# Kernel tuning notes

Measured on AMD Instinct MI355X. Metric: run time of the kernel, lower is better.

Reference implementation:

```python
import jax, jax.numpy as jnp
import numpy as np
from jax.scipy.special import xlogy

NUM_TTA = 64
FILTER_VIEWS = 0.1
KEPT_VIEWS = int(FILTER_VIEWS * NUM_TTA)  # 6
EPS = 1e-8


def setup_inputs() -> dict:
    key = jax.random.key(0)
    k1, k2 = jax.random.split(key)
    x = jax.random.normal(k1, (16384, 4096), dtype=jnp.float32)
    W = jax.random.normal(k2, (4096, 1000), dtype=jnp.float32) * 0.02
    b = jnp.zeros((1000,), dtype=jnp.float32)
    return {"x": x, "W": W, "b": b}


def reference(x, W, b):
    # inner model: linear + softmax -> per-view class probabilities
    probs = jax.nn.softmax(x @ W + b, axis=-1)            # (B*V, C)
    C = probs.shape[-1]
    B = probs.shape[0] // NUM_TTA
    probs = probs.reshape(B, NUM_TTA, C)                  # (b v c)

    # entr(p).sum(-1) == -sum p*log p (entr(0)=0 handled by xlogy)
    entropies = -xlogy(probs, probs).sum(-1)              # (B, V)
    conf_idx = jnp.argsort(entropies, axis=-1)            # most confident first
    votes = jnp.argmax(probs, axis=-1)                    # (B, V)
    sorted_votes = jnp.take_along_axis(votes, conf_idx, axis=1)  # (B, V)

    # initial majority vote over the KEPT_VIEWS most confident views
    counts = jax.nn.one_hot(sorted_votes[:, :KEPT_VIEWS], C, dtype=jnp.float32).sum(1)  # (B, C)

    rows = jnp.arange(B)

    # sequential tie-breaking: while there is a tie at the max, add the next
    # most confident view's vote; at most NUM_TTA - KEPT_VIEWS extra views.
    def body(i, counts):
        maximum = counts.max(axis=-1, keepdims=True)       # (B, 1)
        tied = (counts == maximum).sum(axis=-1) > 1        # (B,)
        cls = sorted_votes[:, KEPT_VIEWS + i]              # (B,)
        return counts.at[rows, cls].add(tied.astype(counts.dtype))

    counts = jax.lax.fori_loop(0, NUM_TTA - KEPT_VIEWS, body, counts)

    predictions = counts / NUM_TTA
    return jnp.log(predictions + EPS)
```

## Files before the change

### kernel.cpp

```cpp
#include <hip/hip_runtime.h>
#include <cstdint>
#include <cstddef>
#include <math.h>

#define M_ROWS 16384
#define N_COLS 1000
#define N_PAD  1024
#define K_DIM  4096
#define NUM_TTA 64
#define KEPT 6
#define BATCH 256
#define CHUNK_MAX 16384
#define NKT (K_DIM / 32)

typedef __attribute__((ext_vector_type(8))) short short8;
typedef __attribute__((ext_vector_type(4))) float v4f;

#define GL_LDS16(g, l)                                                        \
    __builtin_amdgcn_global_load_lds(                                         \
        (const __attribute__((address_space(1))) unsigned int*)(g),           \
        (__attribute__((address_space(3))) unsigned int*)(l), 16, 0, 0)

__device__ __forceinline__ void split2(float x, unsigned short& h, unsigned short& l) {
    const __bf16 hb = (__bf16)x;
    const float hf  = (float)hb;
    const __bf16 lb = (__bf16)(x - hf);
    h = __builtin_bit_cast(unsigned short, hb);
    l = __builtin_bit_cast(unsigned short, lb);
}

__device__ __forceinline__ void split8(const float4& a, const float4& b,
                                       short8& hv, short8& lv) {
    unsigned short h, l;
    split2(a.x, h, l); hv[0] = (short)h; lv[0] = (short)l;
    split2(a.y, h, l); hv[1] = (short)h; lv[1] = (short)l;
    split2(a.z, h, l); hv[2] = (short)h; lv[2] = (short)l;
    split2(a.w, h, l); hv[3] = (short)h; lv[3] = (short)l;
    split2(b.x, h, l); hv[4] = (short)h; lv[4] = (short)l;
    split2(b.y, h, l); hv[5] = (short)h; lv[5] = (short)l;
    split2(b.z, h, l); hv[6] = (short)h; lv[6] = (short)l;
    split2(b.w, h, l); hv[7] = (short)h; lv[7] = (short)l;
}

__global__ __launch_bounds__(1024)
void split_w(const float* __restrict__ W, unsigned short* __restrict__ Wh,
             unsigned short* __restrict__ Wl)
{
    __shared__ float tile[32][33];
    const int k0 = blockIdx.x * 32, n0 = blockIdx.y * 32;
    const int tx = threadIdx.x, ty = threadIdx.y;
    const int n = n0 + tx, k = k0 + ty;
    tile[ty][tx] = (n < N_COLS) ? W[(size_t)k * N_COLS + n] : 0.f;
    __syncthreads();
    const float w = tile[tx][ty];
    unsigned short h, l;
    split2(w, h, l);
    const size_t o = (size_t)(n0 + ty) * K_DIM + k0 + tx;
    Wh[o] = h; Wl[o] = l;
}

__global__ __launch_bounds__(512, 2)
void gemm_mfma(const float* __restrict__ X,
               const unsigned short* __restrict__ Bh_, const unsigned short* __restrict__ Bl_,
               const float* __restrict__ bias, float* __restrict__ logits,
               int m_tiles)
{
    __shared__ __attribute__((aligned(16))) char smem[2 * 4 * 16384];

    const int t    = threadIdx.x;
    const int lane = t & 63;
    const int wave = t >> 6;
    const int wr   = wave >> 2;
    const int wc   = wave & 3;
    const int ml   = lane & 15;
    const int kh   = lane >> 4;

    const int bid  = blockIdx.x;
    const int xcd  = bid & 7;
    const int slot = bid >> 3;
    const int mt   = xcd * (m_tiles >> 3) + (slot >> 2);
    const int nt   = slot & 3;
    const int m0 = mt * 256, n0 = nt * 256;

    const int    schunk = (t & 3) ^ ((t >> 3) & 3);
    const size_t ro     = (size_t)(t >> 2) * (K_DIM * 2) + (size_t)schunk * 16;
    const char* gBh = (const char*)Bh_ + (size_t)n0 * (K_DIM * 2) + ro;
    const char* gBl = (const char*)Bl_ + (size_t)n0 * (K_DIM * 2) + ro;
    char* ldst = smem + t * 16;
    const size_t RSTEP = (size_t)128 * K_DIM * 2;

    const int ar    = t >> 1;
    const int ahalf = t & 1;
    const float* gA = X + (size_t)(m0 + ar) * K_DIM + ahalf * 16;
    const int sig = (ar >> 1) & 3;
    const int s0  = (ahalf * 2) ^ sig;
    const int s1  = (ahalf * 2 + 1) ^ sig;
    const int aw0 = ar * 64 + (s0 << 4);
    const int aw1 = ar * 64 + (s1 << 4);

    const int swz = ((kh ^ (ml >> 1)) & 3) << 4;
    const int lbA = wr * 8192 + ml * 64 + swz;
    const int lbB = wc * 4096 + ml * 64 + swz;

    v4f acc[8][4];
#pragma unroll
    for (int i = 0; i < 8; ++i)
#pragma unroll
        for (int j = 0; j < 4; ++j) acc[i][j] = (v4f){0.f, 0.f, 0.f, 0.f};

#define FRAG(P) (*(const short8*)(smem + (P)))

    short8 ah[4], al[4], bh[4], bl[4];

    {
        const float4 fa = *(const float4*)(gA);
        const float4 fb = *(const float4*)(gA + 4);
        const float4 fc = *(const float4*)(gA + 8);
        const float4 fd = *(const float4*)(gA + 12);
        GL_LDS16(gBh,         ldst + 32768);
        GL_LDS16(gBh + RSTEP, ldst + 40960);
        GL_LDS16(gBl,         ldst + 49152);
        GL_LDS16(gBl + RSTEP, ldst + 57344);
        short8 hv, lv;
        split8(fa, fb, hv, lv);
        *(short8*)(smem + aw0) = hv;
        *(short8*)(smem + 16384 + aw0) = lv;
        split8(fc, fd, hv, lv);
        *(short8*)(smem + aw1) = hv;
        *(short8*)(smem + 16384 + aw1) = lv;
    }
    __syncthreads();

#define TILE_BODY(KT, RB) do {                                                \
    const int B0 = (RB) * 65536;                                              \
    const int B1 = ((RB) ^ 1) * 65536;                                        \
    asm volatile("s_waitcnt vmcnt(0) lgkmcnt(0)" ::: "memory");               \
    __builtin_amdgcn_s_barrier();                                             \
    __builtin_amdgcn_sched_barrier(0);                                        \
    const bool pf = (KT) + 1 < NKT;                                           \
    float4 fa, fb;                                                            \
    if (pf) {       \
        const float* ga_ = gA + ((KT) + 1) * 32;                              \
        fa = *(const float4*)(ga_);                                           \
        fb = *(const float4*)(ga_ + 4);                                       \
        const int kb_ = ((KT) + 1) * 64;                                      \
        GL_LDS16(gBh + kb_,         ldst + B1 + 32768);                       \
        GL_LDS16(gBh + RSTEP + kb_, ldst + B1 + 40960);                       \
        GL_LDS16(gBl + kb_,         ldst + B1 + 49152);                       \
        GL_LDS16(gBl + RSTEP + kb_, ldst + B1 + 57344);                       \
    }                                                                         \
            \
    _Pragma("unroll")                                                         \
    for (int nf = 0; nf < 4; ++nf) {                                          \
        bh[nf] = FRAG(B0 + 32768 + nf * 1024 + lbB);                          \
        bl[nf] = FRAG(B0 + 49152 + nf * 1024 + lbB);                          \
    }                                                                         \
    _Pragma("unroll")                                                         \
    for (int mf = 0; mf < 4; ++mf) {                                          \
        ah[mf] = FRAG(B0 +         mf * 1024 + lbA);                          \
        al[mf] = FRAG(B0 + 16384 + mf * 1024 + lbA);                          \
    }                                                                         \
     \
    __builtin_amdgcn_s_setprio(1);                                            \
    _Pragma("unroll")                                                         \
    for (int mf = 0; mf < 4; ++mf)                                            \
        _Pragma("unroll")                                                     \
        for (int nf = 0; nf < 4; ++nf)                                        \
            acc[mf][nf] = __builtin_amdgcn_mfma_f32_16x16x32_bf16(ah[mf], bl[nf], acc[mf][nf], 0, 0, 0); \
    _Pragma("unroll")                                                         \
    for (int mf = 0; mf < 4; ++mf)                                            \
        _Pragma("unroll")                                                     \
        for (int nf = 0; nf < 4; ++nf)                                        \
            acc[mf][nf] = __builtin_amdgcn_mfma_f32_16x16x32_bf16(al[mf], bh[nf], acc[mf][nf], 0, 0, 0); \
    _Pragma("unroll")                                                         \
    for (int mf = 0; mf < 4; ++mf)                                            \
        _Pragma("unroll")                                                     \
        for (int nf = 0; nf < 4; ++nf)                                        \
            acc[mf][nf] = __builtin_amdgcn_mfma_f32_16x16x32_bf16(ah[mf], bh[nf], acc[mf][nf], 0, 0, 0); \
    __builtin_amdgcn_s_setprio(0);                                            \
    if (pf) {           \
        short8 hv, lv;                                                        \
        split8(fa, fb, hv, lv);                                               \
        *(short8*)(smem + B1 + aw0) = hv;                                     \
        *(short8*)(smem + B1 + 16384 + aw0) = lv;                             \
        const float* ga_ = gA + ((KT) + 1) * 32 + 8;                          \
        fa = *(const float4*)(ga_);                                           \
        fb = *(const float4*)(ga_ + 4);                                       \
    }                                                                         \
      \
    _Pragma("unroll")                                                         \
    for (int mf = 0; mf < 4; ++mf) {                                          \
        ah[mf] = FRAG(B0 + 4096 +         mf * 1024 + lbA);                   \
        al[mf] = FRAG(B0 + 4096 + 16384 + mf * 1024 + lbA);                   \
    }                                                                         \
                      \
    __builtin_amdgcn_s_setprio(1);                                            \
    _Pragma("unroll")                                                         \
    for (int mf = 0; mf < 4; ++mf)                                            \
        _Pragma("unroll")                                                     \
        for (int nf = 0; nf < 4; ++nf)                                        \
            acc[4 + mf][nf] = __builtin_amdgcn_mfma_f32_16x16x32_bf16(ah[mf], bl[nf], acc[4 + mf][nf], 0, 0, 0); \
    _Pragma("unroll")                                                         \
    for (int mf = 0; mf < 4; ++mf)                                            \
        _Pragma("unroll")                                                     \
        for (int nf = 0; nf < 4; ++nf)                                        \
            acc[4 + mf][nf] = __builtin_amdgcn_mfma_f32_16x16x32_bf16(al[mf], bh[nf], acc[4 + mf][nf], 0, 0, 0); \
    _Pragma("unroll")                                                         \
    for (int mf = 0; mf < 4; ++mf)                                            \
        _Pragma("unroll")                                                     \
        for (int nf = 0; nf < 4; ++nf)                                        \
            acc[4 + mf][nf] = __builtin_amdgcn_mfma_f32_16x16x32_bf16(ah[mf], bh[nf], acc[4 + mf][nf], 0, 0, 0); \
    __builtin_amdgcn_s_setprio(0);                                            \
    if (pf) {                                 \
        short8 hv, lv;                                                        \
        split8(fa, fb, hv, lv);                                               \
        *(short8*)(smem + B1 + aw1) = hv;                                     \
        *(short8*)(smem + B1 + 16384 + aw1) = lv;                             \
    }                                                                         \
} while (0)

#pragma unroll 1
    for (int kt = 0; kt < NKT; kt += 2) {
        TILE_BODY(kt, 0);
        TILE_BODY(kt + 1, 1);
    }

#pragma unroll
    for (int mi = 0; mi < 8; ++mi) {
        const int rbase = m0 + wr * 128 + (mi >> 2) * 64 + (mi & 3) * 16 + kh * 4;
#pragma unroll
        for (int ni = 0; ni < 4; ++ni) {
            const int col = n0 + wc * 64 + ni * 16 + ml;
            if (col < N_COLS) {
                const float bv = bias[col];
#pragma unroll
                for (int r = 0; r < 4; ++r)
                    logits[(size_t)(rbase + r) * N_COLS + col] = acc[mi][ni][r] + bv;
            }
        }
    }
#undef TILE_BODY
#undef FRAG
}

__device__ __forceinline__ double exp_neg(double d) {
    if (d < -700.0) return 0.0;
    const double kd = rint(d * 1.4426950408889634074);
    double r = fma(-kd, 6.93147180369123816490e-01, d);
    r = fma(-kd, 1.90821492927058770002e-10, r);
    double p = 2.08767569878680989792e-09;
    p = fma(p, r, 2.50521083854417187751e-08);
    p = fma(p, r, 2.75573192239858906526e-07);
    p = fma(p, r, 2.75573192239858925110e-06);
    p = fma(p, r, 2.48015873015873015873e-05);
    p = fma(p, r, 1.98412698412698412526e-04);
    p = fma(p, r, 1.38888888888888894069e-03);
    p = fma(p, r, 8.33333333333333321769e-03);
    p = fma(p, r, 4.16666666666666643537e-02);
    p = fma(p, r, 1.66666666666666657415e-01);
    p = fma(p, r, 5.0e-01);
    p = fma(p, r, 1.0);
    p = fma(p, r, 1.0);
    const long long k = (long long)kd;
    return p * __longlong_as_double((1023LL + k) << 52);
}

__global__ __launch_bounds__(256)
void row_stats(const float* __restrict__ logits, double* __restrict__ ent,
               int* __restrict__ votes, int v_base)
{
    const int lane = threadIdx.x & 63;
    const int wave = threadIdx.x >> 6;
    const int row  = blockIdx.x * 4 + wave;
    const float* rp = logits + (size_t)row * N_COLS;

    float v[16];
    float bv = -3.0e38f; int bi = 0;
#pragma unroll
    for (int j = 0; j < 16; ++j) {
        const int c = j * 64 + lane;
        const float x = (c < N_COLS) ? rp[c] : -3.0e38f;
        v[j] = x;
        if (x > bv) { bv = x; bi = c; }
    }
#pragma unroll
    for (int s = 32; s > 0; s >>= 1) {
        const float ov = __shfl_xor(bv, s);
        const int   oi = __shfl_xor(bi, s);
        if (ov > bv || (ov == bv && oi < bi)) { bv = ov; bi = oi; }
    }
    const float mx = bv;
    const int amax = bi;

    double S = 0.0, T = 0.0;
#pragma unroll
    for (int j = 0; j < 16; ++j) {
        const int c = j * 64 + lane;
        if (c < N_COLS) {
            const float d = v[j] - mx;
            const double e = exp_neg((double)d);
            S += e; T += e * (double)d;
        }
    }
#pragma unroll
    for (int s = 32; s > 0; s >>= 1) {
        S += __shfl_xor(S, s);
        T += __shfl_xor(T, s);
    }
    if (lane == 0) {
        ent[v_base + row]   = log(S) - T / S;
        votes[v_base + row] = amax;
    }
}

__global__ __launch_bounds__(64)
void vote_kernel(const double* __restrict__ ent, const int* __restrict__ votes,
                 float* __restrict__ out)
{
    __shared__ double e[NUM_TTA];
    __shared__ int    sv[NUM_TTA];
    __shared__ float  counts[N_COLS];

    const int b = blockIdx.x;
    const int t = threadIdx.x;

    e[t] = ent[b * NUM_TTA + t];
    const int myv = votes[b * NUM_TTA + t];
    for (int c = t; c < N_COLS; c += NUM_TTA) counts[c] = 0.f;
    __syncthreads();

    const double et = e[t];
    int rank = 0;
#pragma unroll
    for (int i = 0; i < NUM_TTA; ++i) {
        const double ei = e[i];
        rank += (ei < et) || (ei == et && i < t);
    }
    sv[rank] = myv;
    __syncthreads();

    if (t == 0) {
        for (int j = 0; j < KEPT; ++j) counts[sv[j]] += 1.f;
        float Mv = 0.f; int Tc = 0;
        for (int j = 0; j < KEPT; ++j) {
            const int c = sv[j];
            bool dup = false;
            for (int q = 0; q < j; ++q) dup = dup || (sv[q] == c);
            if (dup) continue;
            const float cv = counts[c];
            if (cv > Mv) { Mv = cv; Tc = 1; }
            else if (cv == Mv) { Tc += 1; }
        }
        for (int i = 0; i < NUM_TTA - KEPT; ++i) {
            if (Tc <= 1) break;
            const int c = sv[KEPT + i];
            const float oldc = counts[c];
            counts[c] = oldc + 1.f;
            if (oldc == Mv)            { Mv += 1.f; Tc = 1; }
            else if (oldc + 1.f == Mv) { Tc += 1; }
        }
    }
    __syncthreads();

    const size_t o0 = (size_t)b * N_COLS;
    for (int c = t; c < N_COLS; c += NUM_TTA)
        out[o0 + c] = logf(counts[c] * (1.f / 64.f) + 1e-8f);
}

extern "C" void kernel_launch(void* const* d_in, const int* in_sizes, int n_in,
                              void* d_out, int out_size, void* d_ws, size_t ws_size,
                              hipStream_t stream) {
    const float* x    = (const float*)d_in[0];
    const float* Wm   = (const float*)d_in[1];
    const float* bias = (const float*)d_in[2];
    float* out = (float*)d_out;

    char* p = (char*)d_ws;
    double* ent  = (double*)p;                     p += (size_t)M_ROWS * 8;
    int*   votes = (int*)p;                        p += (size_t)M_ROWS * 4;
    unsigned short* Wh = (unsigned short*)p;       p += (size_t)N_PAD * K_DIM * 2;
    unsigned short* Wl = (unsigned short*)p;       p += (size_t)N_PAD * K_DIM * 2;
    const size_t base = (size_t)(p - (char*)d_ws);

    long long R = 0;
    if (ws_size > base) R = (long long)((ws_size - base) / (size_t)4000);
    R = (R / 2048) * 2048;
    if (R > CHUNK_MAX) R = CHUNK_MAX;
    if (R < 2048) R = 2048;

    float* logits = (float*)p;

    split_w<<<dim3(K_DIM / 32, N_PAD / 32), dim3(32, 32), 0, stream>>>(Wm, Wh, Wl);

    for (int m0 = 0; m0 < M_ROWS; m0 += (int)R) {
        const int rows = (int)(((long long)(M_ROWS - m0) < R) ? (M_ROWS - m0) : R);
        const int m_tiles = rows / 256;
        gemm_mfma<<<4 * m_tiles, 512, 0, stream>>>(
            x + (size_t)m0 * K_DIM, Wh, Wl, bias, logits, m_tiles);
        row_stats<<<rows / 4, 256, 0, stream>>>(logits, ent, votes, m0);
    }
    vote_kernel<<<BATCH, NUM_TTA, 0, stream>>>(ent, votes, out);
}
```

Baseline: 655.4 us.

## Switch GEMM inner loop to 32x32x16 bf16 MFMA tiles

Replaces the 16x16x32 bf16 MFMA instructions with 32x32x16 variants, so each wave covers the same 128x64 output tile with 4x2 v16f accumulators instead of 8x4 v4f. This needs a new LDS read addressing and swizzle (per-32-lane rows, k-quarter XOR), different fragment reads per k-step and a remapped epilogue store layout. The intent is to cut LDS fragment reads per FLOP and the MFMA issue count by using the larger instruction. The risk is bank conflicts from the new swizzle and a different latency or dependency pattern between the MFMAs.

```diff
diff --git a/kernel.cpp b/kernel.cpp
--- a/kernel.cpp
+++ b/kernel.cpp
@@ -14,7 +14,7 @@
 #define NKT (K_DIM / 32)
 
 typedef __attribute__((ext_vector_type(8))) short short8;
-typedef __attribute__((ext_vector_type(4))) float v4f;
+typedef __attribute__((ext_vector_type(16))) float v16f;
 
 #define GL_LDS16(g, l)                                                        \
     __builtin_amdgcn_global_load_lds(                                         \
@@ -72,8 +72,8 @@
     const int wave = t >> 6;
     const int wr   = wave >> 2;
     const int wc   = wave & 3;
-    const int ml   = lane & 15;
-    const int kh   = lane >> 4;
+    const int l31  = lane & 31;
+    const int kq   = lane >> 5;
 
     const int bid  = blockIdx.x;
     const int xcd  = bid & 7;
@@ -92,25 +92,29 @@
     const int ar    = t >> 1;
     const int ahalf = t & 1;
     const float* gA = X + (size_t)(m0 + ar) * K_DIM + ahalf * 16;
-    const int sig = (ar >> 1) & 3;
-    const int s0  = (ahalf * 2) ^ sig;
-    const int s1  = (ahalf * 2 + 1) ^ sig;
+    const int sigw = (ar >> 1) & 3;
+    const int s0  = (ahalf * 2) ^ sigw;
+    const int s1  = (ahalf * 2 + 1) ^ sigw;
     const int aw0 = ar * 64 + (s0 << 4);
     const int aw1 = ar * 64 + (s1 << 4);
 
-    const int swz = ((kh ^ (ml >> 1)) & 3) << 4;
-    const int lbA = wr * 8192 + ml * 64 + swz;
-    const int lbB = wc * 4096 + ml * 64 + swz;
-
-    v4f acc[8][4];
-#pragma unroll
-    for (int i = 0; i < 8; ++i)
-#pragma unroll
-        for (int j = 0; j < 4; ++j) acc[i][j] = (v4f){0.f, 0.f, 0.f, 0.f};
+    const int sig  = (l31 >> 1) & 3;
+    const int rdsw = ((kq ^ sig) & 3) << 4;
+    const int lbA = wr * 8192 + l31 * 64 + rdsw;
+    const int lbB = wc * 4096 + l31 * 64 + rdsw;
+
+    v16f acc[4][2];
+#pragma unroll
+    for (int i = 0; i < 4; ++i)
+#pragma unroll
+        for (int j = 0; j < 2; ++j)
+#pragma unroll
+            for (int r = 0; r < 16; ++r) acc[i][j][r] = 0.f;
 
 #define FRAG(P) (*(const short8*)(smem + (P)))
-
-    short8 ah[4], al[4], bh[4], bl[4];
+#define SB __builtin_amdgcn_sched_barrier(0)
+
+    short8 ah[4], al[4], bh[2], bl[2];
 
     {
         const float4 fa = *(const float4*)(gA);
@@ -131,12 +135,43 @@
     }
     __syncthreads();
 
+#define RD_KS(XO) do {                                                        \
+    bh[0] = FRAG((B0 + 32768 +        lbB) ^ (XO));                           \
+    bl[0] = FRAG((B0 + 49152 +        lbB) ^ (XO));                           \
+    bh[1] = FRAG((B0 + 32768 + 2048 + lbB) ^ (XO));                           \
+    bl[1] = FRAG((B0 + 49152 + 2048 + lbB) ^ (XO));                           \
+    _Pragma("unroll")                                                         \
+    for (int mf = 0; mf < 4; ++mf) {                                          \
+        ah[mf] = FRAG((B0 +         mf * 2048 + lbA) ^ (XO));                 \
+        al[mf] = FRAG((B0 + 16384 + mf * 2048 + lbA) ^ (XO));                 \
+    }                                                                         \
+} while (0)
+#define MM_KS() do {                                                          \
+    __builtin_amdgcn_s_setprio(1);                                            \
+    _Pragma("unroll")                                                         \
+    for (int mf = 0; mf < 4; ++mf)                                            \
+        _Pragma("unroll")                                                     \
+        for (int nf = 0; nf < 2; ++nf)                                        \
+            acc[mf][nf] = __builtin_amdgcn_mfma_f32_32x32x16_bf16(ah[mf], bl[nf], acc[mf][nf], 0, 0, 0); \
+    _Pragma("unroll")                                                         \
+    for (int mf = 0; mf < 4; ++mf)                                            \
+        _Pragma("unroll")                                                     \
+        for (int nf = 0; nf < 2; ++nf)                                        \
+            acc[mf][nf] = __builtin_amdgcn_mfma_f32_32x32x16_bf16(al[mf], bh[nf], acc[mf][nf], 0, 0, 0); \
+    _Pragma("unroll")                                                         \
+    for (int mf = 0; mf < 4; ++mf)                                            \
+        _Pragma("unroll")                                                     \
+        for (int nf = 0; nf < 2; ++nf)                                        \
+            acc[mf][nf] = __builtin_amdgcn_mfma_f32_32x32x16_bf16(ah[mf], bh[nf], acc[mf][nf], 0, 0, 0); \
+    __builtin_amdgcn_s_setprio(0);                                            \
+} while (0)
+
 #define TILE_BODY(KT, RB) do {                                                \
     const int B0 = (RB) * 65536;                                              \
     const int B1 = ((RB) ^ 1) * 65536;                                        \
     asm volatile("s_waitcnt vmcnt(0) lgkmcnt(0)" ::: "memory");               \
     __builtin_amdgcn_s_barrier();                                             \
-    __builtin_amdgcn_sched_barrier(0);                                        \
+    SB;                                                                       \
     const bool pf = (KT) + 1 < NKT;                                           \
     float4 fa, fb;                                                            \
     if (pf) {       \
@@ -149,35 +184,9 @@
         GL_LDS16(gBl + kb_,         ldst + B1 + 49152);                       \
         GL_LDS16(gBl + RSTEP + kb_, ldst + B1 + 57344);                       \
     }                                                                         \
-            \
-    _Pragma("unroll")                                                         \
-    for (int nf = 0; nf < 4; ++nf) {                                          \
-        bh[nf] = FRAG(B0 + 32768 + nf * 1024 + lbB);                          \
-        bl[nf] = FRAG(B0 + 49152 + nf * 1024 + lbB);                          \
-    }                                                                         \
-    _Pragma("unroll")                                                         \
-    for (int mf = 0; mf < 4; ++mf) {                                          \
-        ah[mf] = FRAG(B0 +         mf * 1024 + lbA);                          \
-        al[mf] = FRAG(B0 + 16384 + mf * 1024 + lbA);                          \
-    }                                                                         \
-     \
-    __builtin_amdgcn_s_setprio(1);                                            \
-    _Pragma("unroll")                                                         \
-    for (int mf = 0; mf < 4; ++mf)                                            \
-        _Pragma("unroll")                                                     \
-        for (int nf = 0; nf < 4; ++nf)                                        \
-            acc[mf][nf] = __builtin_amdgcn_mfma_f32_16x16x32_bf16(ah[mf], bl[nf], acc[mf][nf], 0, 0, 0); \
-    _Pragma("unroll")                                                         \
-    for (int mf = 0; mf < 4; ++mf)                                            \
-        _Pragma("unroll")                                                     \
-        for (int nf = 0; nf < 4; ++nf)                                        \
-            acc[mf][nf] = __builtin_amdgcn_mfma_f32_16x16x32_bf16(al[mf], bh[nf], acc[mf][nf], 0, 0, 0); \
-    _Pragma("unroll")                                                         \
-    for (int mf = 0; mf < 4; ++mf)                                            \
-        _Pragma("unroll")                                                     \
-        for (int nf = 0; nf < 4; ++nf)                                        \
-            acc[mf][nf] = __builtin_amdgcn_mfma_f32_16x16x32_bf16(ah[mf], bh[nf], acc[mf][nf], 0, 0, 0); \
-    __builtin_amdgcn_s_setprio(0);                                            \
+                                                      \
+    RD_KS(0); SB;                                                             \
+    MM_KS(); SB;                                                              \
     if (pf) {           \
         short8 hv, lv;                                                        \
         split8(fa, fb, hv, lv);                                               \
@@ -187,30 +196,10 @@
         fa = *(const float4*)(ga_);                                           \
         fb = *(const float4*)(ga_ + 4);                                       \
     }                                                                         \
-      \
-    _Pragma("unroll")                                                         \
-    for (int mf = 0; mf < 4; ++mf) {                                          \
-        ah[mf] = FRAG(B0 + 4096 +         mf * 1024 + lbA);                   \
-        al[mf] = FRAG(B0 + 4096 + 16384 + mf * 1024 + lbA);                   \
-    }                                                                         \
-                      \
-    __builtin_amdgcn_s_setprio(1);                                            \
-    _Pragma("unroll")                                                         \
-    for (int mf = 0; mf < 4; ++mf)                                            \
-        _Pragma("unroll")                                                     \
-        for (int nf = 0; nf < 4; ++nf)                                        \
-            acc[4 + mf][nf] = __builtin_amdgcn_mfma_f32_16x16x32_bf16(ah[mf], bl[nf], acc[4 + mf][nf], 0, 0, 0); \
-    _Pragma("unroll")                                                         \
-    for (int mf = 0; mf < 4; ++mf)                                            \
-        _Pragma("unroll")                                                     \
-        for (int nf = 0; nf < 4; ++nf)                                        \
-            acc[4 + mf][nf] = __builtin_amdgcn_mfma_f32_16x16x32_bf16(al[mf], bh[nf], acc[4 + mf][nf], 0, 0, 0); \
-    _Pragma("unroll")                                                         \
-    for (int mf = 0; mf < 4; ++mf)                                            \
-        _Pragma("unroll")                                                     \
-        for (int nf = 0; nf < 4; ++nf)                                        \
-            acc[4 + mf][nf] = __builtin_amdgcn_mfma_f32_16x16x32_bf16(ah[mf], bh[nf], acc[4 + mf][nf], 0, 0, 0); \
-    __builtin_amdgcn_s_setprio(0);                                            \
+    SB;                                                                       \
+          \
+    RD_KS(0x20); SB;                                                          \
+    MM_KS(); SB;                                                              \
     if (pf) {                                 \
         short8 hv, lv;                                                        \
         split8(fa, fb, hv, lv);                                               \
@@ -226,20 +215,25 @@
     }
 
 #pragma unroll
-    for (int mi = 0; mi < 8; ++mi) {
-        const int rbase = m0 + wr * 128 + (mi >> 2) * 64 + (mi & 3) * 16 + kh * 4;
-#pragma unroll
-        for (int ni = 0; ni < 4; ++ni) {
-            const int col = n0 + wc * 64 + ni * 16 + ml;
+    for (int mf = 0; mf < 4; ++mf) {
+        const int rbase = m0 + wr * 128 + mf * 32 + kq * 4;
+#pragma unroll
+        for (int nf = 0; nf < 2; ++nf) {
+            const int col = n0 + wc * 64 + nf * 32 + l31;
             if (col < N_COLS) {
                 const float bv = bias[col];
 #pragma unroll
-                for (int r = 0; r < 4; ++r)
-                    logits[(size_t)(rbase + r) * N_COLS + col] = acc[mi][ni][r] + bv;
+                for (int r = 0; r < 16; ++r) {
+                    const int row = rbase + (r & 3) + 8 * (r >> 2);
+                    logits[(size_t)row * N_COLS + col] = acc[mf][nf][r] + bv;
+                }
             }
         }
     }
 #undef TILE_BODY
+#undef MM_KS
+#undef RD_KS
+#undef SB
 #undef FRAG
 }
 
```

Result: slower. 685.3 us (+4.5%).
